# Kernel optimization log

Hardware: AMD Instinct MI355X
Metric: run time of the kernel (lower is better)

The kernel has to match this reference:

```python
import jax, jax.numpy as jnp
from jax import lax
import numpy as np

B = 32  # batch


def _conv(x, w, b, pad):
    # x: [B,Cin,H,W], w: [Cout,Cin,kh,kw], b: [Cout]
    y = lax.conv_general_dilated(x, w, window_strides=(1, 1), padding=pad,
                                 dimension_numbers=("NCHW", "OIHW", "NCHW"))
    return y + b[None, :, None, None]


def setup_inputs() -> dict:
    keys = jax.random.split(jax.random.key(0), 16)
    ki = iter(keys)
    f32 = jnp.float32

    def W(shape):
        return jax.random.normal(next(ki), shape, f32) * 0.05

    return {
        "x": jax.random.normal(next(ki), (B, 64, 64), f32),
        # 64 independent spatial convs per stage, each Conv2d(Cin,31,(64,3))
        "W1": W((64, 31, 1, 64, 3)),  "b1": jnp.zeros((64, 31), f32),
        "W2": W((64, 31, 31, 64, 3)), "b2": jnp.zeros((64, 31), f32),
        "W3": W((64, 31, 31, 64, 3)), "b3": jnp.zeros((64, 31), f32),
        # 2 edge spectral stacks: Conv(2,64,9)->ReLU->Conv(64,32,1)->ReLU->Conv(32,1,5)
        "We1a": W((2, 64, 2, 9, 9)),  "be1a": jnp.zeros((2, 64), f32),
        "We1b": W((2, 32, 64, 1, 1)), "be1b": jnp.zeros((2, 32), f32),
        "We1c": W((2, 1, 32, 5, 5)),  "be1c": jnp.zeros((2, 1), f32),
        # 29 interior spectral stacks: Conv(3,64,9)->ReLU->Conv(64,32,1)->ReLU->Conv(32,1,5)
        "We2a": W((29, 64, 3, 9, 9)),  "be2a": jnp.zeros((29, 64), f32),
        "We2b": W((29, 32, 64, 1, 1)), "be2b": jnp.zeros((29, 32), f32),
        "We2c": W((29, 1, 32, 5, 5)),  "be2c": jnp.zeros((29, 1), f32),
    }


def _spatial(inp, Ws, bs):
    # inp: [B,Cin,64,64]; Ws: [64,31,Cin,64,3]; bs: [64,31]
    def one(w, b):
        return jax.nn.relu(_conv(inp, w, b, [(0, 0), (1, 1)]))  # [B,31,1,64]
    rows = jax.vmap(one)(Ws, bs)            # [64,B,31,1,64]; row i = output line i
    return jnp.transpose(rows[:, :, :, 0, :], (1, 2, 0, 3))  # [B,31,64,64]


def _spectral(xin, wa, ba, wb, bb, wc, bc):
    h = jax.nn.relu(_conv(xin, wa, ba, [(4, 4), (4, 4)]))
    h = jax.nn.relu(_conv(h, wb, bb, [(0, 0), (0, 0)]))
    return _conv(h, wc, bc, [(2, 2), (2, 2)])[:, 0]  # [B,64,64]


def reference(x, W1, b1, W2, b2, W3, b3,
              We1a, be1a, We1b, be1b, We1c, be1c,
              We2a, be2a, We2b, be2b, We2c, be2c):
    xb = x[:, None]                         # [B,1,64,64]
    s1 = _spatial(xb, W1, b1)               # [B,31,64,64]
    s2 = _spatial(s1, W2, b2)
    s3 = _spatial(s2, W3, b3)

    # edge bands 0 and 30 use 2-channel slices
    edge_in = jnp.stack([s3[:, 0:2], s3[:, 29:31]])   # [2,B,2,64,64]
    edge = jax.vmap(_spectral)(edge_in, We1a, be1a, We1b, be1b, We1c, be1c)  # [2,B,64,64]

    # interior bands 1..29 use sliding 3-channel slices
    idx = jnp.arange(29)[:, None] + jnp.arange(3)[None, :]  # [29,3]
    mid_in = jnp.transpose(s3[:, idx], (1, 0, 2, 3, 4))     # [29,B,3,64,64]
    mid = jax.vmap(_spectral)(mid_in, We2a, be2a, We2b, be2b, We2c, be2c)  # [29,B,64,64]

    recon = jnp.concatenate(
        [edge[0][:, None], jnp.transpose(mid, (1, 0, 2, 3)), edge[1][:, None]], axis=1)
    out = s3 + recon                        # [B,31,64,64]
    # torch: .transpose(3,1).transpose(2,1) == permute(0,2,3,1)
    return jnp.transpose(out, (0, 2, 3, 1))  # [B,64,64,31]
```

## Files before the change

### kernel.cpp

```cpp
#include <hip/hip_runtime.h>
#include <hip/hip_bf16.h>
#include <stdint.h>

typedef unsigned short u16;
typedef unsigned int   u32;
typedef __attribute__((ext_vector_type(8))) short bf16x8;
typedef __attribute__((ext_vector_type(4))) float f32x4;

__device__ __forceinline__ float us2f(u16 u){ return __uint_as_float(((u32)u)<<16); }
__device__ __forceinline__ float lo2f(u32 w){ return __uint_as_float(w<<16); }
__device__ __forceinline__ float hi2f(u32 w){ return __uint_as_float(w & 0xffff0000u); }
__device__ __forceinline__ u16 f2us(float f){
  u32 u = __float_as_uint(f);
  u32 r = (u + 0x7FFFu + ((u>>16)&1u)) >> 16;
  return (u16)r;
}
__device__ __forceinline__ u32 pk2(float a, float b){ return (u32)f2us(a) | ((u32)f2us(b)<<16); }

__global__ __launch_bounds__(256) void k_prep_x(const float* __restrict__ x, u16* __restrict__ xT){
  __shared__ float tile[64][65];
  const int b = blockIdx.x, t = threadIdx.x;
  #pragma unroll
  for (int q=0;q<4;q++){
    int idx = q*256 + t, r = idx>>4, w4 = (idx&15)*4;
    float4 v = *(const float4*)&x[((size_t)b*64 + r)*64 + w4];
    tile[r][w4]=v.x; tile[r][w4+1]=v.y; tile[r][w4+2]=v.z; tile[r][w4+3]=v.w;
  }
  __syncthreads();
  #pragma unroll
  for (int q=0;q<2;q++){
    int idx = q*256 + t, w = idx>>3, rc = idx&7;
    uint4 o;
    o.x = pk2(tile[rc*8+0][w], tile[rc*8+1][w]);
    o.y = pk2(tile[rc*8+2][w], tile[rc*8+3][w]);
    o.z = pk2(tile[rc*8+4][w], tile[rc*8+5][w]);
    o.w = pk2(tile[rc*8+6][w], tile[rc*8+7][w]);
    *(uint4*)&xT[((size_t)b*64 + w)*64 + rc*8] = o;
  }
}

__global__ __launch_bounds__(256) void k_prep_w(const float* __restrict__ W,
        u16* __restrict__ Wp, int CI){
  __shared__ float rowW[5952];
  const int h = blockIdx.x, i = blockIdx.y, t = threadIdx.x;
  for (int idx=t; idx<1488; idx+=256){
    int o = idx/48, j4 = (idx - o*48)*4;
    float4 v = *(const float4*)&W[ (((size_t)h*31 + o)*CI + i)*192 + j4 ];
    *(float4*)&rowW[o*192 + j4] = v;
  }
  __syncthreads();
  for (int idx=t; idx<768; idx+=256){
    int dw = idx>>8, rem = idx&255, o = rem>>3, rc = rem&7;
    uint4 ov = {0,0,0,0};
    if (o < 31){
      const float* s = &rowW[o*192 + dw];
      ov.x = pk2(s[(rc*8+0)*3], s[(rc*8+1)*3]);
      ov.y = pk2(s[(rc*8+2)*3], s[(rc*8+3)*3]);
      ov.z = pk2(s[(rc*8+4)*3], s[(rc*8+5)*3]);
      ov.w = pk2(s[(rc*8+6)*3], s[(rc*8+7)*3]);
    }
    *(uint4*)&Wp[ ((((size_t)h*CI + i)*3 + dw)*32 + o)*64 + rc*8 ] = ov;
  }
}

__global__ __launch_bounds__(256) void k_spatial2(const u16* __restrict__ inT_g,
        const u16* __restrict__ Wp, const float* __restrict__ bias,
        float* __restrict__ outF, u16* __restrict__ outT, int CI, int mode){
  __shared__ __align__(16) u16 inT[2][34*72];
  const int t    = threadIdx.x;
  const int wv   = t>>6;
  const int lane = t&63;
  const int l15  = lane&15;
  const int quad = lane>>4;
  const int wg  = blockIdx.x;
  const int xcd = wg & 7;
  const int li  = wg >> 3;
  const int hg  = xcd*2 + (li>>6);
  const int sub = li & 63;
  const int b   = sub >> 1;
  const int whalf = sub & 1;
  const int h  = hg*4 + wv;
  const int w0 = whalf*32;

  f32x4 acc[2][2];
  #pragma unroll
  for (int n=0;n<2;n++)
    #pragma unroll
    for (int ms=0;ms<2;ms++) acc[n][ms] = (f32x4){0.f,0.f,0.f,0.f};

  for (int i=0;i<CI;i++){
    u16* L = inT[i&1];
    const uint4* src = (const uint4*)(inT_g + (size_t)(b*CI + i)*4096);
    #pragma unroll
    for (int q=0;q<2;q++){
      int idx = q*256 + t;
      if (idx < 272){
        int row = idx>>3, ch = idx&7;
        int gw = w0 - 1 + row;
        uint4 v = {0,0,0,0};
        if (gw >= 0 && gw < 64) v = src[gw*8 + ch];
        *(uint4*)&L[row*72 + ch*8] = v;
      }
    }
    const u16* wbase = Wp + ((size_t)h*CI + i)*3*32*64;
    bf16x8 bfr[2][3][2];
    #pragma unroll
    for (int dw=0;dw<3;dw++)
      #pragma unroll
      for (int n=0;n<2;n++)
        #pragma unroll
        for (int kh=0;kh<2;kh++)
          bfr[kh][dw][n] = *(const bf16x8*)&wbase[(dw*32 + n*16 + l15)*64 + kh*32 + quad*8];
    __syncthreads();
    #pragma unroll
    for (int kh=0; kh<2; kh++){
      #pragma unroll
      for (int dw=0; dw<3; dw++){
        bf16x8 afr[2];
        #pragma unroll
        for (int ms=0;ms<2;ms++)
          afr[ms] = *(const bf16x8*)&L[(ms*16 + l15 + dw)*72 + kh*32 + quad*8];
        #pragma unroll
        for (int n=0;n<2;n++)
          #pragma unroll
          for (int ms=0;ms<2;ms++)
            acc[n][ms] = __builtin_amdgcn_mfma_f32_16x16x32_bf16(afr[ms], bfr[kh][dw][n], acc[n][ms], 0,0,0);
      }
    }
  }
  #pragma unroll
  for (int n=0;n<2;n++){
    int o = n*16 + l15;
    if (o < 31){
      float bv = bias[h*31 + o];
      if (mode == 0){
        #pragma unroll
        for (int ms=0;ms<2;ms++){
          size_t base = (((size_t)b*31 + o)*64 + h)*64 + w0 + ms*16 + quad*4;
          #pragma unroll
          for (int reg=0;reg<4;reg++)
            outF[base + reg] = fmaxf(acc[n][ms][reg] + bv, 0.f);
        }
      } else {
        #pragma unroll
        for (int ms=0;ms<2;ms++){
          int ww = w0 + ms*16 + quad*4;
          #pragma unroll
          for (int reg=0;reg<4;reg++)
            outT[ (((size_t)b*31 + o)*64 + (ww+reg))*64 + h ] = f2us(fmaxf(acc[n][ms][reg] + bv, 0.f));
        }
      }
    }
  }
}

__global__ __launch_bounds__(256) void k_prep(
    const float* __restrict__ We1a, const float* __restrict__ We2a,
    const float* __restrict__ We1b, const float* __restrict__ We2b,
    u16* __restrict__ waP, u16* __restrict__ wbP){
  int t = blockIdx.x*256 + threadIdx.x;
  if (t < 17856){
    int g = t/576, rem = t - g*576, dx = rem>>6, c = rem&63;
    int C; const float* wa;
    if (g==0)      { C=2; wa = We1a; }
    else if (g==30){ C=2; wa = We1a + 64*2*81; }
    else           { C=3; wa = We2a + (size_t)(g-1)*64*3*81; }
    const float* wrow = wa + (size_t)c*C*81;
    u16* dst = waP + ((size_t)(g*9 + dx)*64 + c)*40;
    int Kr = C*9;
    for (int k=0;k<40;k++){
      u16 v = 0;
      if (k < Kr) v = f2us(wrow[k*9 + dx]);
      dst[k] = v;
    }
  } else if (t < 17856 + 992){
    int u = t - 17856; int g = u>>5, c2 = u&31;
    const float* wb;
    if (g==0)      wb = We1b;
    else if (g==30) wb = We1b + 32*64;
    else            wb = We2b + (size_t)(g-1)*32*64;
    u16* dst = wbP + ((size_t)g*32 + c2)*72;
    for (int k=0;k<64;k++) dst[k] = f2us(wb[c2*64 + k]);
    for (int k=64;k<72;k++) dst[k] = 0;
  }
}

__global__ __launch_bounds__(256) void k_spec_ab(
    const float* __restrict__ s3,
    const u16* __restrict__ waP, const u16* __restrict__ wbP,
    const float* __restrict__ be1a, const float* __restrict__ be1b,
    const float* __restrict__ be2a, const float* __restrict__ be2b,
    u16* __restrict__ hb, int g0){
  __shared__ __align__(16) unsigned char smem[36864];
  u16* colT = (u16*)smem;
  u16* haT  = (u16*)smem;
  u16* hbL  = (u16*)smem;

  const int t = threadIdx.x;
  const int yo = blockIdx.x, b = blockIdx.y;
  const int gl = blockIdx.z;
  const int g  = g0 + gl;
  const int y0 = yo*4;
  const int wv = t>>6, lane = t&63, l15 = lane&15, quad = lane>>4;

  int C, cb; const float *ba, *bb;
  if (g==0)      { C=2; cb=0;  ba=be1a;           bb=be1b;        }
  else if (g==30){ C=2; cb=29; ba=be1a+64;        bb=be1b+32;     }
  else           { C=3; cb=g-1; ba=be2a+(size_t)(g-1)*64; bb=be2b+(size_t)(g-1)*32; }

  {
    uint4 z = {0,0,0,0};
    uint4* c4 = (uint4*)colT;
    #pragma unroll
    for (int j=0;j<6;j++){ int idx = j*256 + t; if (idx < 1440) c4[idx] = z; }
  }
  __syncthreads();

  for (int idx=t; idx<576; idx+=256){
    int i = idx/192, rem = idx-192*i;
    int x4 = rem/12, yext = rem - x4*12;
    int yrow = y0 + yext - 4;
    if (i < C && yrow >= 0 && yrow < 64){
      float4 v = *(const float4*)&s3[ (((size_t)b*31 + cb + i)*64 + yrow)*64 + x4*4 ];
      u16 q0=f2us(v.x), q1=f2us(v.y), q2=f2us(v.z), q3=f2us(v.w);
      #pragma unroll
      for (int yl=0; yl<4; yl++){
        int dy = yext - yl;
        if (dy >= 0 && dy < 9){
          int k = i*9 + dy;
          int base = (yl*72 + x4*4 + 4)*40 + k;
          colT[base      ] = q0;
          colT[base + 40 ] = q1;
          colT[base + 80 ] = q2;
          colT[base + 120] = q3;
        }
      }
    }
  }
  __syncthreads();

  f32x4 acc[4][4];
  #pragma unroll
  for (int yl=0;yl<4;yl++)
    #pragma unroll
    for (int nf=0;nf<4;nf++) acc[yl][nf] = (f32x4){0.f,0.f,0.f,0.f};

  const u16* waPg = waP + (size_t)g*9*64*40;
  #pragma unroll
  for (int dx=0; dx<9; dx++){
    bf16x8 af[4];
    #pragma unroll
    for (int yl=0;yl<4;yl++)
      af[yl] = *(const bf16x8*)&colT[(yl*72 + wv*16 + l15 + dx)*40 + quad*8];
    #pragma unroll
    for (int nf=0;nf<4;nf++){
      bf16x8 bfr = *(const bf16x8*)&waPg[(dx*64 + nf*16 + l15)*40 + quad*8];
      #pragma unroll
      for (int yl=0;yl<4;yl++)
        acc[yl][nf] = __builtin_amdgcn_mfma_f32_16x16x32_bf16(af[yl], bfr, acc[yl][nf], 0,0,0);
    }
  }
  __syncthreads();

  #pragma unroll
  for (int nf=0;nf<4;nf++){
    float bav = ba[nf*16 + l15];
    #pragma unroll
    for (int yl=0;yl<4;yl++){
      int px = yl*64 + wv*16 + quad*4;
      #pragma unroll
      for (int reg=0;reg<4;reg++)
        haT[(px+reg)*72 + nf*16 + l15] = f2us(fmaxf(acc[yl][nf][reg] + bav, 0.f));
    }
  }
  __syncthreads();

  bf16x8 a2[2][4];
  #pragma unroll
  for (int kh=0; kh<2; kh++)
    #pragma unroll
    for (int j=0;j<4;j++)
      a2[kh][j] = *(const bf16x8*)&haT[((wv*4+j)*16 + l15)*72 + kh*32 + quad*8];
  __syncthreads();

  const u16* wb_g = wbP + (size_t)g*32*72;
  f32x4 acc2[4][2];
  #pragma unroll
  for (int j=0;j<4;j++){ acc2[j][0] = (f32x4){0.f,0.f,0.f,0.f}; acc2[j][1] = (f32x4){0.f,0.f,0.f,0.f}; }
  #pragma unroll
  for (int kh=0; kh<2; kh++){
    #pragma unroll
    for (int nf=0;nf<2;nf++){
      bf16x8 b2 = *(const bf16x8*)&wb_g[(nf*16 + l15)*72 + kh*32 + quad*8];
      #pragma unroll
      for (int j=0;j<4;j++)
        acc2[j][nf] = __builtin_amdgcn_mfma_f32_16x16x32_bf16(a2[kh][j], b2, acc2[j][nf], 0,0,0);
    }
  }
  #pragma unroll
  for (int nf=0;nf<2;nf++){
    float bbv = bb[nf*16 + l15];
    #pragma unroll
    for (int j=0;j<4;j++){
      int px = (wv*4+j)*16 + quad*4;
      uint2 pw;
      pw.x = pk2(fmaxf(acc2[j][nf][0] + bbv, 0.f), fmaxf(acc2[j][nf][1] + bbv, 0.f));
      pw.y = pk2(fmaxf(acc2[j][nf][2] + bbv, 0.f), fmaxf(acc2[j][nf][3] + bbv, 0.f));
      *(uint2*)&hbL[(nf*16+l15)*296 + px] = pw;
    }
  }
  __syncthreads();

  {
    int c2 = t>>3, xq = t&7;
    size_t base = (((size_t)gl*32 + b)*32 + c2)*4096 + (size_t)yo*256 + xq*32;
    #pragma unroll
    for (int q=0;q<4;q++)
      *(uint4*)&hb[base + q*8] = *(const uint4*)&hbL[c2*296 + xq*32 + q*8];
  }
}

__global__ __launch_bounds__(256) void k_spec_c(
    const u16* __restrict__ hb, const float* __restrict__ We1c, const float* __restrict__ be1c,
    const float* __restrict__ We2c, const float* __restrict__ be2c,
    float* __restrict__ rec, int g0){
  __shared__ __align__(16) unsigned char smemC[58368 + 3200];
  u16*   hbT  = (u16*)smemC;
  float* wcL  = (float*)(smemC + 58368);
  float* redc = (float*)smemC;
  const int t  = threadIdx.x;
  const int y0 = blockIdx.x*8;
  const int b  = blockIdx.y;
  const int gl = blockIdx.z;
  const int g  = g0 + gl;
  const float *wc, *bc;
  if (g==0)      { wc = We1c;             bc = be1c;       }
  else if (g==30){ wc = We1c + 800;       bc = be1c + 1;   }
  else           { wc = We2c + (g-1)*800; bc = be2c + (g-1); }

  for (int idx=t; idx<384; idx+=256){
    int c2 = idx/12, row = idx - c2*12;
    u32* d32 = (u32*)&hbT[(size_t)(c2*12 + row)*76];
    d32[0]  = 0;
    d32[33] = 0;
    u32* di = d32 + 1;
    int yg = y0 - 2 + row;
    if (yg >= 0 && yg < 64){
      const uint4* srcp = (const uint4*)&hb[ (((size_t)gl*32 + b)*32 + c2)*4096 + (size_t)yg*64 ];
      #pragma unroll
      for (int q=0;q<8;q++){
        uint4 v = srcp[q];
        di[q*4+0]=v.x; di[q*4+1]=v.y; di[q*4+2]=v.z; di[q*4+3]=v.w;
      }
    } else {
      #pragma unroll
      for (int q=0;q<32;q++) di[q] = 0;
    }
  }
  for (int idx=t; idx<800; idx+=256) wcL[idx] = wc[idx];
  __syncthreads();

  const int xt = t&7, yq = (t>>3)&7, cqt = t>>6;
  const int x0 = xt*8;
  float acc[8];
  #pragma unroll
  for (int p=0;p<8;p++) acc[p]=0.f;
  for (int c2 = cqt*8; c2 < cqt*8+8; c2++){
    #pragma unroll
    for (int dy=0;dy<5;dy++){
      const uint2* hp = (const uint2*)&hbT[(c2*12 + yq+dy)*76 + x0];
      uint2 v0 = hp[0], v1 = hp[1], v2 = hp[2];
      float h[12];
      h[0]=lo2f(v0.x); h[1]=hi2f(v0.x); h[2]=lo2f(v0.y); h[3]=hi2f(v0.y);
      h[4]=lo2f(v1.x); h[5]=hi2f(v1.x); h[6]=lo2f(v1.y); h[7]=hi2f(v1.y);
      h[8]=lo2f(v2.x); h[9]=hi2f(v2.x); h[10]=lo2f(v2.y); h[11]=hi2f(v2.y);
      #pragma unroll
      for (int dx=0;dx<5;dx++){
        float wv = wcL[c2*25 + dy*5 + dx];
        #pragma unroll
        for (int p=0;p<8;p++) acc[p] = fmaf(h[p+dx], wv, acc[p]);
      }
    }
  }
  __syncthreads();
  int slot = yq*8 + xt;
  if (cqt >= 2){
    #pragma unroll
    for (int p=0;p<8;p++) redc[((cqt-2)*64 + slot)*8 + p] = acc[p];
  }
  __syncthreads();
  if (cqt < 2){
    #pragma unroll
    for (int p=0;p<8;p++) acc[p] += redc[(cqt*64 + slot)*8 + p];
  }
  __syncthreads();
  if (cqt == 1){
    #pragma unroll
    for (int p=0;p<8;p++) redc[slot*8 + p] = acc[p];
  }
  __syncthreads();
  if (cqt == 0){
    float bcv = bc[0];
    size_t base = (((size_t)g*32 + b)*64 + (y0+yq))*64 + x0;
    #pragma unroll
    for (int p=0;p<8;p++) rec[base+p] = acc[p] + redc[slot*8 + p] + bcv;
  }
}

__global__ __launch_bounds__(256) void k_final(const float* __restrict__ s3,
        const float* __restrict__ rec, float* __restrict__ out){
  __shared__ float tile[31][65];
  const int t = threadIdx.x;
  const int y = blockIdx.x & 63;
  const int b = blockIdx.x >> 6;
  for (int idx=t; idx<1984; idx+=256){
    int o = idx>>6, x = idx&63;
    tile[o][x] = s3[ (((size_t)b*31+o)*64 + y)*64 + x ]
               + rec[ (((size_t)o*32+b)*64 + y)*64 + x ];
  }
  __syncthreads();
  size_t base = ((size_t)b*4096 + (size_t)y*64)*31;
  for (int idx=t; idx<1984; idx+=256){
    int x = idx/31, o = idx-31*x;
    out[base+idx] = tile[o][x];
  }
}

extern "C" void kernel_launch(void* const* d_in, const int* in_sizes, int n_in,
                              void* d_out, int out_size, void* d_ws, size_t ws_size,
                              hipStream_t stream){
  const float* x    = (const float*)d_in[0];
  const float* W1   = (const float*)d_in[1];
  const float* b1   = (const float*)d_in[2];
  const float* W2   = (const float*)d_in[3];
  const float* b2   = (const float*)d_in[4];
  const float* W3   = (const float*)d_in[5];
  const float* b3   = (const float*)d_in[6];
  const float* We1a = (const float*)d_in[7];
  const float* be1a = (const float*)d_in[8];
  const float* We1b = (const float*)d_in[9];
  const float* be1b = (const float*)d_in[10];
  const float* We1c = (const float*)d_in[11];
  const float* be1c = (const float*)d_in[12];
  const float* We2a = (const float*)d_in[13];
  const float* be2a = (const float*)d_in[14];
  const float* We2b = (const float*)d_in[15];
  const float* be2b = (const float*)d_in[16];
  const float* We2c = (const float*)d_in[17];
  const float* be2c = (const float*)d_in[18];
  float* out = (float*)d_out;

  char* ws = (char*)d_ws;
  float* s3  = (float*)(ws);
  u16*   Wp  = (u16*)(ws + 16777216);
  u16*   xT  = (u16*)(ws + 44040192);
  float* rec = (float*)(ws + 16777216);
  u16*   hb  = (u16*)(ws + 33030144);

  u16* s1T = (u16*)((char*)d_out);
  u16* s2T = (u16*)((char*)d_out + 8126464);
  u16* waP = (u16*)((char*)d_out);
  u16* wbP = (u16*)((char*)d_out + 1440000);

  dim3 bs(256);
  k_prep_x<<<dim3(32),bs,0,stream>>>(x, xT);
  k_prep_w<<<dim3(64,1),bs,0,stream>>>(W1, Wp, 1);
  k_spatial2<<<dim3(1024),bs,0,stream>>>(xT,  Wp, b1, nullptr, s1T, 1, 1);
  k_prep_w<<<dim3(64,31),bs,0,stream>>>(W2, Wp, 31);
  k_spatial2<<<dim3(1024),bs,0,stream>>>(s1T, Wp, b2, nullptr, s2T, 31, 1);
  k_prep_w<<<dim3(64,31),bs,0,stream>>>(W3, Wp, 31);
  k_spatial2<<<dim3(1024),bs,0,stream>>>(s2T, Wp, b3, s3, nullptr, 31, 0);

  k_prep<<<dim3(74),bs,0,stream>>>(We1a, We2a, We1b, We2b, waP, wbP);

  int batch = 8;
  if (ws_size > 33030144ull){
    size_t m = (ws_size - 33030144ull) / 8388608ull;
    if (m < 1) m = 1;
    if (m > 8) m = 8;
    batch = (int)m;
  }
  for (int g0=0; g0<31; g0+=batch){
    int c = 31 - g0; if (c > batch) c = batch;
    k_spec_ab<<<dim3(16,32,c),bs,0,stream>>>(s3, waP, wbP, be1a, be1b, be2a, be2b, hb, g0);
    k_spec_c <<<dim3(8,32,c),bs,0,stream>>>(hb, We1c,be1c,We2c,be2c, rec, g0);
  }
  k_final<<<dim3(2048),bs,0,stream>>>(s3, rec, out);
}
```

Measured before the change: 1.136 ms.

## Retile spatial conv to full-width rows with register prefetch of input channels

The spatial conv kernel now uses 128-thread blocks. Each block covers one batch and two output rows, and each wave covers the full 64-wide row instead of a 32-wide half, so the input tile is loaded once per channel rather than twice with halo. The next channel's input is prefetched into registers while the current one is computed, and zero padding rows are written once at start. The full __syncthreads is replaced by an lgkmcnt wait plus a raw barrier. In exchange each wave holds more accumulators, raising register use, and the block count changes to 1024 blocks of 2 waves, which shifts occupancy and drops the previous XCD-aware mapping.

```diff
diff --git a/kernel.cpp b/kernel.cpp
--- a/kernel.cpp
+++ b/kernel.cpp
@@ -63,44 +63,47 @@
   }
 }
 
-__global__ __launch_bounds__(256) void k_spatial2(const u16* __restrict__ inT_g,
+__global__ __launch_bounds__(128) void k_spatial2(const u16* __restrict__ inT_g,
         const u16* __restrict__ Wp, const float* __restrict__ bias,
         float* __restrict__ outF, u16* __restrict__ outT, int CI, int mode){
-  __shared__ __align__(16) u16 inT[2][34*72];
+  __shared__ __align__(16) u16 inT[2][66*72];
   const int t    = threadIdx.x;
   const int wv   = t>>6;
   const int lane = t&63;
   const int l15  = lane&15;
   const int quad = lane>>4;
-  const int wg  = blockIdx.x;
-  const int xcd = wg & 7;
-  const int li  = wg >> 3;
-  const int hg  = xcd*2 + (li>>6);
-  const int sub = li & 63;
-  const int b   = sub >> 1;
-  const int whalf = sub & 1;
-  const int h  = hg*4 + wv;
-  const int w0 = whalf*32;
-
-  f32x4 acc[2][2];
+  const int b    = blockIdx.x;
+  const int hg   = blockIdx.y;
+  const int h    = hg*2 + wv;
+
+  if (t < 72){
+    inT[0][t] = 0; inT[0][65*72 + t] = 0;
+    inT[1][t] = 0; inT[1][65*72 + t] = 0;
+  }
+
+  f32x4 acc[2][4];
   #pragma unroll
   for (int n=0;n<2;n++)
     #pragma unroll
-    for (int ms=0;ms<2;ms++) acc[n][ms] = (f32x4){0.f,0.f,0.f,0.f};
+    for (int ms=0;ms<4;ms++) acc[n][ms] = (f32x4){0.f,0.f,0.f,0.f};
+
+  const uint4* srcb = (const uint4*)(inT_g + (size_t)b*CI*4096);
+
+  uint4 pf[4];
+  #pragma unroll
+  for (int q=0;q<4;q++) pf[q] = srcb[q*128 + t];
 
   for (int i=0;i<CI;i++){
     u16* L = inT[i&1];
-    const uint4* src = (const uint4*)(inT_g + (size_t)(b*CI + i)*4096);
-    #pragma unroll
-    for (int q=0;q<2;q++){
-      int idx = q*256 + t;
-      if (idx < 272){
-        int row = idx>>3, ch = idx&7;
-        int gw = w0 - 1 + row;
-        uint4 v = {0,0,0,0};
-        if (gw >= 0 && gw < 64) v = src[gw*8 + ch];
-        *(uint4*)&L[row*72 + ch*8] = v;
-      }
+    #pragma unroll
+    for (int q=0;q<4;q++){
+      int idx = q*128 + t, row = idx>>3, ch = idx&7;
+      *(uint4*)&L[(row+1)*72 + ch*8] = pf[q];
+    }
+    if (i+1 < CI){
+      const uint4* src = srcb + (size_t)(i+1)*512;
+      #pragma unroll
+      for (int q=0;q<4;q++) pf[q] = src[q*128 + t];
     }
     const u16* wbase = Wp + ((size_t)h*CI + i)*3*32*64;
     bf16x8 bfr[2][3][2];
@@ -111,19 +114,21 @@
         #pragma unroll
         for (int kh=0;kh<2;kh++)
           bfr[kh][dw][n] = *(const bf16x8*)&wbase[(dw*32 + n*16 + l15)*64 + kh*32 + quad*8];
-    __syncthreads();
+    asm volatile("s_waitcnt lgkmcnt(0)" ::: "memory");
+    __builtin_amdgcn_s_barrier();
+    __builtin_amdgcn_sched_barrier(0);
     #pragma unroll
     for (int kh=0; kh<2; kh++){
       #pragma unroll
       for (int dw=0; dw<3; dw++){
-        bf16x8 afr[2];
-        #pragma unroll
-        for (int ms=0;ms<2;ms++)
+        bf16x8 afr[4];
+        #pragma unroll
+        for (int ms=0;ms<4;ms++)
           afr[ms] = *(const bf16x8*)&L[(ms*16 + l15 + dw)*72 + kh*32 + quad*8];
         #pragma unroll
         for (int n=0;n<2;n++)
           #pragma unroll
-          for (int ms=0;ms<2;ms++)
+          for (int ms=0;ms<4;ms++)
             acc[n][ms] = __builtin_amdgcn_mfma_f32_16x16x32_bf16(afr[ms], bfr[kh][dw][n], acc[n][ms], 0,0,0);
       }
     }
@@ -135,19 +140,19 @@
       float bv = bias[h*31 + o];
       if (mode == 0){
         #pragma unroll
-        for (int ms=0;ms<2;ms++){
-          size_t base = (((size_t)b*31 + o)*64 + h)*64 + w0 + ms*16 + quad*4;
+        for (int ms=0;ms<4;ms++){
+          size_t base = (((size_t)b*31 + o)*64 + h)*64 + ms*16 + quad*4;
           #pragma unroll
           for (int reg=0;reg<4;reg++)
             outF[base + reg] = fmaxf(acc[n][ms][reg] + bv, 0.f);
         }
       } else {
         #pragma unroll
-        for (int ms=0;ms<2;ms++){
-          int ww = w0 + ms*16 + quad*4;
+        for (int ms=0;ms<4;ms++){
+          int w0 = ms*16 + quad*4;
           #pragma unroll
           for (int reg=0;reg<4;reg++)
-            outT[ (((size_t)b*31 + o)*64 + (ww+reg))*64 + h ] = f2us(fmaxf(acc[n][ms][reg] + bv, 0.f));
+            outT[ (((size_t)b*31 + o)*64 + (w0+reg))*64 + h ] = f2us(fmaxf(acc[n][ms][reg] + bv, 0.f));
         }
       }
     }
@@ -463,13 +468,14 @@
   u16* wbP = (u16*)((char*)d_out + 1440000);
 
   dim3 bs(256);
+  dim3 bsp(128), gsp(32,32);
   k_prep_x<<<dim3(32),bs,0,stream>>>(x, xT);
   k_prep_w<<<dim3(64,1),bs,0,stream>>>(W1, Wp, 1);
-  k_spatial2<<<dim3(1024),bs,0,stream>>>(xT,  Wp, b1, nullptr, s1T, 1, 1);
+  k_spatial2<<<gsp,bsp,0,stream>>>(xT,  Wp, b1, nullptr, s1T, 1, 1);
   k_prep_w<<<dim3(64,31),bs,0,stream>>>(W2, Wp, 31);
-  k_spatial2<<<dim3(1024),bs,0,stream>>>(s1T, Wp, b2, nullptr, s2T, 31, 1);
+  k_spatial2<<<gsp,bsp,0,stream>>>(s1T, Wp, b2, nullptr, s2T, 31, 1);
   k_prep_w<<<dim3(64,31),bs,0,stream>>>(W3, Wp, 31);
-  k_spatial2<<<dim3(1024),bs,0,stream>>>(s2T, Wp, b3, s3, nullptr, 31, 0);
+  k_spatial2<<<gsp,bsp,0,stream>>>(s2T, Wp, b3, s3, nullptr, 31, 0);
 
   k_prep<<<dim3(74),bs,0,stream>>>(We1a, We2a, We1b, We2b, waP, wbP);
 
```

After: 1.043 ms. -8.2%, faster.
